# Kernel tuning notes

Measured on AMD Instinct MI355X. Metric: run time of the kernel, lower is better.

Reference implementation:

```python
import jax, jax.numpy as jnp
import numpy as np

B, D_IN, D_HID, D_OUT, N_EXP, K = 32768, 256, 512, 256, 16, 2


def setup_inputs() -> dict:
    key = jax.random.key(0)
    ks = jax.random.split(key, 5)
    s_in = 1.0 / np.sqrt(D_IN)
    s_hid = 1.0 / np.sqrt(D_HID)
    return {
        "x": jax.random.normal(ks[0], (B, D_IN), jnp.float32),
        "Wg": jax.random.normal(ks[1], (D_IN, N_EXP), jnp.float32) * s_in,
        "bg": jnp.zeros((N_EXP,), jnp.float32),
        "W1": jax.random.normal(ks[2], (N_EXP, D_IN, D_HID), jnp.float32) * s_in,
        "b1": jnp.zeros((N_EXP, D_HID), jnp.float32),
        "W2": jax.random.normal(ks[3], (N_EXP, D_HID, D_OUT), jnp.float32) * s_hid,
        "b2": jnp.zeros((N_EXP, D_OUT), jnp.float32),
    }


def reference(x, Wg, bg, W1, b1, W2, b2):
    # Gating: linear -> softmax -> top-k -> renormalize (inference path, no noise)
    logits = x @ Wg + bg                       # [B, E]
    probs = jax.nn.softmax(logits, axis=-1)
    top_w, top_idx = jax.lax.top_k(probs, K)   # [B, K]
    top_w = top_w / jnp.sum(top_w, axis=-1, keepdims=True)

    # Expert MLPs (evaluate all experts densely, then gather selected outputs;
    # same math as masked gather -> MLP -> weighted scatter-add)
    h = jax.nn.relu(jnp.einsum('bi,eih->beh', x, W1) + b1[None])  # [B, E, H]
    y_all = jnp.einsum('beh,eho->beo', h, W2) + b2[None]          # [B, E, O]

    y_sel = jnp.take_along_axis(y_all, top_idx[:, :, None], axis=1)  # [B, K, O]
    return jnp.sum(y_sel * top_w[:, :, None], axis=1)                # [B, O]
```

## Files before the change

### kernel.cpp

```cpp
#include <hip/hip_runtime.h>
#include <stdint.h>

#define BTOK 32768
#define DIN 256
#define DHID 512
#define DOUT 256
#define NEXP 16
#define BM 128
#define CH 64
#define NCH 8
#define SLOTS 96

typedef __attribute__((ext_vector_type(8))) short bf16x8;
typedef __attribute__((ext_vector_type(16))) float f32x16;

__device__ __forceinline__ unsigned short f2bf(float f){
  unsigned u = __builtin_bit_cast(unsigned, f);
  u = u + 0x7FFFu + ((u >> 16) & 1u);
  return (unsigned short)(u >> 16);
}
__device__ __forceinline__ float bf2f(unsigned short h){
  return __builtin_bit_cast(float, (unsigned)h << 16);
}
__device__ __forceinline__ void gload16(const void* g, void* l){
  __builtin_amdgcn_global_load_lds((const __attribute__((address_space(1))) unsigned int*)g,
                                   (__attribute__((address_space(3))) unsigned int*)l, 16, 0, 0);
}

__global__ __launch_bounds__(256) void transpose_cvt(const float* __restrict__ src,
                                                     unsigned short* __restrict__ dst,
                                                     int R, int C){
  __shared__ float t[32][33];
  int e = blockIdx.z, r0 = blockIdx.y * 32, c0 = blockIdx.x * 32;
  int lx = threadIdx.x & 31, ly = threadIdx.x >> 5;
  const float* s = src + (size_t)e * R * C;
  unsigned short* d = dst + (size_t)e * R * C;
#pragma unroll
  for (int i = 0; i < 4; i++){ int r = ly + i * 8; t[r][lx] = s[(size_t)(r0 + r) * C + c0 + lx]; }
  __syncthreads();
#pragma unroll
  for (int i = 0; i < 4; i++){ int r = ly + i * 8; d[(size_t)(c0 + r) * R + r0 + lx] = f2bf(t[lx][r]); }
}

__global__ __launch_bounds__(256) void transpose_cvt_w2(const float* __restrict__ src,
                                                        unsigned short* __restrict__ dst){
  __shared__ float t[32][33];
  int e = blockIdx.z, r0 = blockIdx.y * 32, c0 = blockIdx.x * 32;
  int lx = threadIdx.x & 31, ly = threadIdx.x >> 5;
  const float* s = src + (size_t)e * DHID * DOUT;
  unsigned short* d = dst + (size_t)e * DHID * DOUT + (r0 >> 6) * (DOUT * CH) + (r0 & 32);
#pragma unroll
  for (int i = 0; i < 4; i++){ int r = ly + i * 8; t[r][lx] = s[(size_t)(r0 + r) * DOUT + c0 + lx]; }
  __syncthreads();
#pragma unroll
  for (int i = 0; i < 4; i++){ int rr = ly + i * 8; d[(size_t)(c0 + rr) * CH + lx] = f2bf(t[lx][rr]); }
}

__global__ __launch_bounds__(256) void gating_kernel(const float* __restrict__ x,
                                                     const float* __restrict__ Wg,
                                                     const float* __restrict__ bg,
                                                     unsigned short* __restrict__ x_bf,
                                                     int* __restrict__ top_idx,
                                                     float* __restrict__ top_w,
                                                     int* __restrict__ counts){
  __shared__ float WgT[16][256];
  __shared__ int hist[16];
  int tid = threadIdx.x;
#pragma unroll
  for (int j = 0; j < 4; j++){
    float4 wv = *(const float4*)(Wg + tid * 16 + j * 4);
    WgT[j * 4 + 0][tid] = wv.x; WgT[j * 4 + 1][tid] = wv.y;
    WgT[j * 4 + 2][tid] = wv.z; WgT[j * 4 + 3][tid] = wv.w;
  }
  if (tid < 16) hist[tid] = 0;
  __syncthreads();
  int wid = tid >> 6, lane = tid & 63;

  for (int t = 0; t < 16; t++){
    int tok = blockIdx.x * 64 + wid * 16 + t;
    const float4 xv = *(const float4*)(x + (size_t)tok * DIN + lane * 4);
    ushort4 xb; xb.x = f2bf(xv.x); xb.y = f2bf(xv.y); xb.z = f2bf(xv.z); xb.w = f2bf(xv.w);
    *(ushort4*)(x_bf + (size_t)tok * DIN + lane * 4) = xb;
    float logit[16];
#pragma unroll
    for (int e = 0; e < 16; e++){
      const float4 wv = *(const float4*)(&WgT[e][lane * 4]);
      float v = xv.x * wv.x + xv.y * wv.y + xv.z * wv.z + xv.w * wv.w;
#pragma unroll
      for (int off = 32; off; off >>= 1) v += __shfl_xor(v, off, 64);
      logit[e] = v + bg[e];
    }
    if (lane == 0){
      int i1 = 0; float v1 = logit[0];
#pragma unroll
      for (int e = 1; e < 16; e++) if (logit[e] > v1){ v1 = logit[e]; i1 = e; }
      int i2 = -1; float v2 = -3.4e38f;
#pragma unroll
      for (int e = 0; e < 16; e++) if (e != i1 && logit[e] > v2){ v2 = logit[e]; i2 = e; }
      float tt = expf(v2 - v1);
      float w1 = 1.0f / (1.0f + tt);
      float w2 = tt / (1.0f + tt);
      top_idx[tok * 2] = i1; top_idx[tok * 2 + 1] = i2;
      top_w[tok * 2] = w1;  top_w[tok * 2 + 1] = w2;
      atomicAdd(&hist[i1], 1); atomicAdd(&hist[i2], 1);
    }
  }
  __syncthreads();
  if (tid < 16) atomicAdd(&counts[tid], hist[tid]);
}

__global__ void prefix_kernel(const int* __restrict__ counts, int* __restrict__ offsets,
                              int* __restrict__ cursor, int* __restrict__ bm_e,
                              int* __restrict__ bm_start, int* __restrict__ bm_end,
                              int* __restrict__ xcd_cnt, int* __restrict__ xcd_cur){
  int lane = threadIdx.x & 63;
  int c = (lane < 16) ? counts[lane] : 0;
  int s = c;
#pragma unroll
  for (int off = 1; off < 16; off <<= 1){ int o = __shfl_up(s, off, 64); if (lane >= off) s += o; }
  int start = s - c;
  if (lane < 16){ offsets[lane] = start; cursor[lane] = start; }
  int nb = (c + BM - 1) >> 7;
  int nb_partner = __shfl(nb, lane ^ 8, 64);
  if (lane < 8){
    int filled = nb + nb_partner;
    if (filled > SLOTS) filled = SLOTS;
    xcd_cnt[lane] = filled;
    xcd_cur[lane] = 0;
  }
  if (lane < 16){
    int sbase = (lane < 8) ? 0 : nb_partner;
    int xcd = lane & 7;
    for (int b = 0; b < nb; b++){
      int idx = xcd * SLOTS + sbase + b;
      if (sbase + b < SLOTS){
        bm_e[idx] = lane; bm_start[idx] = start + b * BM; bm_end[idx] = start + c;
      }
    }
  }
}

__global__ __launch_bounds__(256) void scatter_kernel(const int* __restrict__ top_idx,
                                                      const float* __restrict__ top_w,
                                                      int* __restrict__ cursor,
                                                      int* __restrict__ pair_tok,
                                                      float* __restrict__ pair_w){
  __shared__ int hist[16], base[16], rank[16];
  int tid = threadIdx.x;
  if (tid < 16){ hist[tid] = 0; rank[tid] = 0; }
  __syncthreads();
  int t = blockIdx.x * 256 + tid;
  int e0 = top_idx[t * 2], e1 = top_idx[t * 2 + 1];
  float w0 = top_w[t * 2], w1 = top_w[t * 2 + 1];
  atomicAdd(&hist[e0], 1); atomicAdd(&hist[e1], 1);
  __syncthreads();
  if (tid < 16) base[tid] = atomicAdd(&cursor[tid], hist[tid]);
  __syncthreads();
  int r0 = atomicAdd(&rank[e0], 1);
  int p0 = base[e0] + r0;
  pair_tok[p0] = t; pair_w[p0] = w0;
  int r1 = atomicAdd(&rank[e1], 1);
  int p1 = base[e1] + r1;
  pair_tok[p1] = t | (1 << 16); pair_w[p1] = w1;
}

__global__ __launch_bounds__(512, 1) void moe_gemm_kernel(
    const unsigned short* __restrict__ x_bf,
    const unsigned short* __restrict__ W1t,
    const unsigned short* __restrict__ W2c,
    const float* __restrict__ b1,
    const float* __restrict__ b2,
    const int* __restrict__ pair_tok, const float* __restrict__ pair_w,
    const int* __restrict__ bm_e, const int* __restrict__ bm_start,
    const int* __restrict__ bm_end,
    int* __restrict__ xcd_cur, const int* __restrict__ xcd_cnt,
    unsigned short* __restrict__ ypair){
  int xcd = blockIdx.x & 7;

  __shared__ unsigned short w1s[2][CH * 256];
  __shared__ unsigned short w2s[2][256 * CH];
  __shared__ unsigned short hs[BM * CH];
  __shared__ int s_u;

  int tid = threadIdx.x, wid = tid >> 6, lane = tid & 63;
  int l31 = lane & 31, l5 = lane >> 5;
  int mg = wid >> 1, hg = wid & 1;
  char* hsb = (char*)hs;

  int o1, o2;
  { int r = tid >> 5; o1 = r * 512 + (((tid & 31) ^ (r & 15)) * 16); }
  { int p = tid >> 4; int q = (tid & 15) ^ (p & 15);
    o2 = (p * 2 + (q >> 3)) * 128 + (q & 7) * 16; }

  int hid = hg * 32 + l31;
  int swzA = (hid & 15) << 4;
  const f32x16 fzero = {0.f,0.f,0.f,0.f,0.f,0.f,0.f,0.f,0.f,0.f,0.f,0.f,0.f,0.f,0.f,0.f};
  int cnt = xcd_cnt[xcd];

  for (;;){
    if (tid == 0) s_u = atomicAdd(&xcd_cur[xcd], 1);
    __syncthreads();
    int u = s_u;
    if (u >= cnt) break;
    int bmi = xcd * SLOTS + u;
    int e = bm_e[bmi], rs = bm_start[bmi], re = bm_end[bmi];
    const char* gW1 = (const char*)(W1t + (size_t)e * DHID * DIN);
    const char* gW2 = (const char*)(W2c + (size_t)e * DOUT * DHID);

#define STAGE(c, sl) {                                                    \
    const char* s1 = gW1 + (size_t)(c) * 32768;                           \
    const char* s2 = gW2 + (size_t)(c) * 32768;                           \
    char* d1 = (char*)w1s[sl]; char* d2 = (char*)w2s[sl];                 \
    _Pragma("unroll")                                                     \
    for (int k = 0; k < 4; k++){                                          \
      gload16(s1 + o1 + k * 8192, d1 + tid * 16 + k * 8192);              \
      gload16(s2 + o2 + k * 8192, d2 + tid * 16 + k * 8192);              \
    } }

    bf16x8 xr[16];
    {
      int g0 = rs + mg * 32 + l31;
      int gc = g0 < re ? g0 : (re - 1);
      int tok = pair_tok[gc] & 0xFFFF;
      const unsigned short* xrow = x_bf + (size_t)tok * DIN + l5 * 8;
#pragma unroll
      for (int ks = 0; ks < 16; ks++) xr[ks] = *(const bf16x8*)(xrow + ks * 16);
    }

    f32x16 acc[4];
    acc[0] = fzero; acc[1] = fzero; acc[2] = fzero; acc[3] = fzero;

    STAGE(0, 0);
    asm volatile("s_waitcnt vmcnt(0)" ::: "memory");
    __builtin_amdgcn_sched_barrier(0);
    __builtin_amdgcn_s_barrier();
    __builtin_amdgcn_sched_barrier(0);

    for (int c = 0; c < NCH; c++){
      int sl = c & 1;
      if (c + 1 < NCH) STAGE(c + 1, sl ^ 1);

      float b1v = b1[e * DHID + c * CH + hid];

      {
        const char* w1b = (const char*)w1s[sl];
        f32x16 h0 = fzero, h1 = fzero;
#pragma unroll
        for (int ks = 0; ks < 16; ks += 2){
          bf16x8 bA = *(const bf16x8*)(w1b + hid * 512 + ((ks * 32 + l5 * 16) ^ swzA));
          bf16x8 bB = *(const bf16x8*)(w1b + hid * 512 + (((ks + 1) * 32 + l5 * 16) ^ swzA));
          h0 = __builtin_amdgcn_mfma_f32_32x32x16_bf16(xr[ks], bA, h0, 0, 0, 0);
          h1 = __builtin_amdgcn_mfma_f32_32x32x16_bf16(xr[ks + 1], bB, h1, 0, 0, 0);
        }
        f32x16 hsum = h0 + h1;
        int h2 = hg * 64 + l31 * 2;
#pragma unroll
        for (int r = 0; r < 16; r++){
          int tk = mg * 32 + (r & 3) + ((r >> 2) << 3) + (l5 << 2);
          float v = fmaxf(hsum[r] + b1v, 0.f);
          int adr = (tk >> 1) * 256 + ((((tk & 1) << 7) + h2) ^ (((tk >> 1) & 15) << 4));
          *(unsigned short*)(hsb + adr) = f2bf(v);
        }
      }
      asm volatile("s_waitcnt lgkmcnt(0)" ::: "memory");
      __builtin_amdgcn_sched_barrier(0);
      __builtin_amdgcn_s_barrier();
      __builtin_amdgcn_sched_barrier(0);

      {
        const char* w2b = (const char*)w2s[sl];
        int tk = mg * 32 + l31;
        int hswz = ((tk >> 1) & 15) << 4;
        int hbase = (tk >> 1) * 256;
        int hhi = (tk & 1) << 7;
#pragma unroll
        for (int ks = 0; ks < 4; ks++){
          bf16x8 ha = *(const bf16x8*)(hsb + hbase + ((hhi + ks * 32 + l5 * 16) ^ hswz));
#pragma unroll
          for (int ot = 0; ot < 4; ot++){
            int n = hg * 128 + ot * 32 + l31;
            int adr = (n >> 1) * 256 + ((((n & 1) << 7) + ks * 32 + l5 * 16) ^ (((n >> 1) & 15) << 4));
            bf16x8 bb = *(const bf16x8*)(w2b + adr);
            acc[ot] = __builtin_amdgcn_mfma_f32_32x32x16_bf16(ha, bb, acc[ot], 0, 0, 0);
          }
        }
      }
      if (c + 1 < NCH){
        asm volatile("s_waitcnt vmcnt(0) lgkmcnt(0)" ::: "memory");
        __builtin_amdgcn_sched_barrier(0);
        __builtin_amdgcn_s_barrier();
        __builtin_amdgcn_sched_barrier(0);
      }
    }

    {
      float b2v[4];
#pragma unroll
      for (int ot = 0; ot < 4; ot++) b2v[ot] = b2[e * DOUT + hg * 128 + ot * 32 + l31];
#pragma unroll
      for (int r = 0; r < 16; r++){
        int tl = mg * 32 + (r & 3) + ((r >> 2) << 3) + (l5 << 2);
        int gg = rs + tl;
        if (gg < re){
          int pt = pair_tok[gg];
          int yrow = (pt & 0xFFFF) * 2 + (pt >> 16);
          float w = pair_w[gg];
          unsigned short* yp = ypair + (size_t)yrow * DOUT + hg * 128 + l31;
#pragma unroll
          for (int ot = 0; ot < 4; ot++)
            yp[ot * 32] = f2bf(w * (acc[ot][r] + b2v[ot]));
        }
      }
    }
#undef STAGE
  }
}

__global__ __launch_bounds__(256) void combine_kernel(const unsigned short* __restrict__ yp,
                                                      float* __restrict__ out){
  int idx = blockIdx.x * 256 + threadIdx.x;
  int t = idx >> 6;
  int c4 = (idx & 63) << 2;
  ushort4 a = *(const ushort4*)(yp + (size_t)(t * 2) * DOUT + c4);
  ushort4 b = *(const ushort4*)(yp + (size_t)(t * 2 + 1) * DOUT + c4);
  float4 o;
  o.x = bf2f(a.x) + bf2f(b.x);
  o.y = bf2f(a.y) + bf2f(b.y);
  o.z = bf2f(a.z) + bf2f(b.z);
  o.w = bf2f(a.w) + bf2f(b.w);
  *(float4*)(out + (size_t)t * DOUT + c4) = o;
}

extern "C" void kernel_launch(void* const* d_in, const int* in_sizes, int n_in,
                              void* d_out, int out_size, void* d_ws, size_t ws_size,
                              hipStream_t stream){
  (void)in_sizes; (void)n_in; (void)out_size; (void)ws_size;
  const float* x  = (const float*)d_in[0];
  const float* Wg = (const float*)d_in[1];
  const float* bg = (const float*)d_in[2];
  const float* W1 = (const float*)d_in[3];
  const float* b1 = (const float*)d_in[4];
  const float* W2 = (const float*)d_in[5];
  const float* b2 = (const float*)d_in[6];
  float* out = (float*)d_out;
  char* ws = (char*)d_ws;

  unsigned short* x_bf  = (unsigned short*)(ws);
  unsigned short* W1t   = (unsigned short*)(ws + 16777216);
  unsigned short* W2ck  = (unsigned short*)(ws + 20971520);
  unsigned short* ypair = (unsigned short*)(ws + 25165824);
  int*   top_idx  = (int*)  (ws + 58720256);
  float* top_w    = (float*)(ws + 58982400);
  int*   pair_tok = (int*)  (ws + 59244544);
  float* pair_w   = (float*)(ws + 59506688);
  int*   counts   = (int*)  (ws + 60030976);
  int*   offsets  = (int*)  (ws + 60031040);
  int*   cursor   = (int*)  (ws + 60031104);
  int*   bm_e     = (int*)  (ws + 60031232);
  int*   bm_start = (int*)  (ws + 60036608);
  int*   bm_end   = (int*)  (ws + 60041984);
  int*   xcd_cnt  = (int*)  (ws + 60045184);
  int*   xcd_cur  = (int*)  (ws + 60045248);

  hipMemsetAsync(counts, 0, 64, stream);
  transpose_cvt<<<dim3(16, 8, 16), 256, 0, stream>>>(W1, W1t, 256, 512);
  transpose_cvt_w2<<<dim3(8, 16, 16), 256, 0, stream>>>(W2, W2ck);
  gating_kernel<<<512, 256, 0, stream>>>(x, Wg, bg, x_bf, top_idx, top_w, counts);
  prefix_kernel<<<1, 64, 0, stream>>>(counts, offsets, cursor, bm_e, bm_start, bm_end,
                                      xcd_cnt, xcd_cur);
  scatter_kernel<<<128, 256, 0, stream>>>(top_idx, top_w, cursor, pair_tok, pair_w);
  moe_gemm_kernel<<<256, 512, 0, stream>>>(x_bf, W1t, W2ck, b1, b2, pair_tok, pair_w,
                                           bm_e, bm_start, bm_end, xcd_cur, xcd_cnt, ypair);
  combine_kernel<<<8192, 256, 0, stream>>>(ypair, out);
}
```

Baseline: 158.5 us.

## Halve hidden chunk size and run two 256-thread blocks per CU in MoE GEMM

Shrinks the hidden-dimension chunk from 64 to 32 (16 chunks instead of 8), halving the LDS used by the weight and hidden staging buffers so two 256-thread blocks can share a CU. Each wave now owns a full 32-token row group and all 256 output columns, which doubles its output accumulators to 8 MFMA tiles. The W2 pre-layout and the LDS swizzles are reworked for the 32-wide chunk, and b1 is cached once per block in LDS. The trade-off is more barriers per tile and higher register pressure, in exchange for more resident waves to overlap latency.

```diff
diff --git a/kernel.cpp b/kernel.cpp
--- a/kernel.cpp
+++ b/kernel.cpp
@@ -7,8 +7,8 @@
 #define DOUT 256
 #define NEXP 16
 #define BM 128
-#define CH 64
-#define NCH 8
+#define CH 32
+#define NCH 16
 #define SLOTS 96
 
 typedef __attribute__((ext_vector_type(8))) short bf16x8;
@@ -48,7 +48,7 @@
   int e = blockIdx.z, r0 = blockIdx.y * 32, c0 = blockIdx.x * 32;
   int lx = threadIdx.x & 31, ly = threadIdx.x >> 5;
   const float* s = src + (size_t)e * DHID * DOUT;
-  unsigned short* d = dst + (size_t)e * DHID * DOUT + (r0 >> 6) * (DOUT * CH) + (r0 & 32);
+  unsigned short* d = dst + (size_t)e * DHID * DOUT + (r0 >> 5) * (DOUT * CH);
 #pragma unroll
   for (int i = 0; i < 4; i++){ int r = ly + i * 8; t[r][lx] = s[(size_t)(r0 + r) * DOUT + c0 + lx]; }
   __syncthreads();
@@ -164,7 +164,7 @@
   pair_tok[p1] = t | (1 << 16); pair_w[p1] = w1;
 }
 
-__global__ __launch_bounds__(512, 1) void moe_gemm_kernel(
+__global__ __launch_bounds__(256, 2) void moe_gemm_kernel(
     const unsigned short* __restrict__ x_bf,
     const unsigned short* __restrict__ W1t,
     const unsigned short* __restrict__ W2c,
@@ -180,19 +180,15 @@
   __shared__ unsigned short w1s[2][CH * 256];
   __shared__ unsigned short w2s[2][256 * CH];
   __shared__ unsigned short hs[BM * CH];
+  __shared__ float b1s[DHID];
   __shared__ int s_u;
 
   int tid = threadIdx.x, wid = tid >> 6, lane = tid & 63;
   int l31 = lane & 31, l5 = lane >> 5;
-  int mg = wid >> 1, hg = wid & 1;
+  int mg = wid;
   char* hsb = (char*)hs;
 
-  int o1, o2;
-  { int r = tid >> 5; o1 = r * 512 + (((tid & 31) ^ (r & 15)) * 16); }
-  { int p = tid >> 4; int q = (tid & 15) ^ (p & 15);
-    o2 = (p * 2 + (q >> 3)) * 128 + (q & 7) * 16; }
-
-  int hid = hg * 32 + l31;
+  int hid = l31;
   int swzA = (hid & 15) << 4;
   const f32x16 fzero = {0.f,0.f,0.f,0.f,0.f,0.f,0.f,0.f,0.f,0.f,0.f,0.f,0.f,0.f,0.f,0.f};
   int cnt = xcd_cnt[xcd];
@@ -208,14 +204,22 @@
     const char* gW2 = (const char*)(W2c + (size_t)e * DOUT * DHID);
 
 #define STAGE(c, sl) {                                                    \
-    const char* s1 = gW1 + (size_t)(c) * 32768;                           \
-    const char* s2 = gW2 + (size_t)(c) * 32768;                           \
+    const char* s1 = gW1 + (size_t)(c) * 16384;                           \
+    const char* s2 = gW2 + (size_t)(c) * 16384;                           \
     char* d1 = (char*)w1s[sl]; char* d2 = (char*)w2s[sl];                 \
     _Pragma("unroll")                                                     \
     for (int k = 0; k < 4; k++){                                          \
-      gload16(s1 + o1 + k * 8192, d1 + tid * 16 + k * 8192);              \
-      gload16(s2 + o2 + k * 8192, d2 + tid * 16 + k * 8192);              \
+      int g = k * 256 + tid;                                              \
+      int r_ = g >> 5;                                                    \
+      int of1 = r_ * 512 + (((g & 31) ^ (r_ & 15)) * 16);                 \
+      int p_ = g >> 3, q_ = (g & 7) ^ (p_ & 7);                           \
+      int of2 = (p_ * 2 + (q_ >> 2)) * 64 + (q_ & 3) * 16;                \
+      gload16(s1 + of1, d1 + g * 16);                                     \
+      gload16(s2 + of2, d2 + g * 16);                                     \
     } }
+
+    b1s[tid] = b1[e * DHID + tid];
+    b1s[tid + 256] = b1[e * DHID + 256 + tid];
 
     bf16x8 xr[16];
     {
@@ -227,8 +231,9 @@
       for (int ks = 0; ks < 16; ks++) xr[ks] = *(const bf16x8*)(xrow + ks * 16);
     }
 
-    f32x16 acc[4];
-    acc[0] = fzero; acc[1] = fzero; acc[2] = fzero; acc[3] = fzero;
+    f32x16 acc[8];
+#pragma unroll
+    for (int i = 0; i < 8; i++) acc[i] = fzero;
 
     STAGE(0, 0);
     asm volatile("s_waitcnt vmcnt(0)" ::: "memory");
@@ -239,8 +244,6 @@
     for (int c = 0; c < NCH; c++){
       int sl = c & 1;
       if (c + 1 < NCH) STAGE(c + 1, sl ^ 1);
-
-      float b1v = b1[e * DHID + c * CH + hid];
 
       {
         const char* w1b = (const char*)w1s[sl];
@@ -253,12 +256,12 @@
           h1 = __builtin_amdgcn_mfma_f32_32x32x16_bf16(xr[ks + 1], bB, h1, 0, 0, 0);
         }
         f32x16 hsum = h0 + h1;
-        int h2 = hg * 64 + l31 * 2;
+        float b1v = b1s[c * CH + l31];
 #pragma unroll
         for (int r = 0; r < 16; r++){
           int tk = mg * 32 + (r & 3) + ((r >> 2) << 3) + (l5 << 2);
           float v = fmaxf(hsum[r] + b1v, 0.f);
-          int adr = (tk >> 1) * 256 + ((((tk & 1) << 7) + h2) ^ (((tk >> 1) & 15) << 4));
+          int adr = (tk >> 1) * 128 + ((((tk & 1) << 6) + l31 * 2) ^ (((tk >> 1) & 7) << 4));
           *(unsigned short*)(hsb + adr) = f2bf(v);
         }
       }
@@ -270,18 +273,19 @@
       {
         const char* w2b = (const char*)w2s[sl];
         int tk = mg * 32 + l31;
-        int hswz = ((tk >> 1) & 15) << 4;
-        int hbase = (tk >> 1) * 256;
-        int hhi = (tk & 1) << 7;
-#pragma unroll
-        for (int ks = 0; ks < 4; ks++){
-          bf16x8 ha = *(const bf16x8*)(hsb + hbase + ((hhi + ks * 32 + l5 * 16) ^ hswz));
-#pragma unroll
-          for (int ot = 0; ot < 4; ot++){
-            int n = hg * 128 + ot * 32 + l31;
-            int adr = (n >> 1) * 256 + ((((n & 1) << 7) + ks * 32 + l5 * 16) ^ (((n >> 1) & 15) << 4));
-            bf16x8 bb = *(const bf16x8*)(w2b + adr);
-            acc[ot] = __builtin_amdgcn_mfma_f32_32x32x16_bf16(ha, bb, acc[ot], 0, 0, 0);
+        int hb = (tk >> 1) * 128, hswz = ((tk >> 1) & 7) << 4, hhi = (tk & 1) << 6;
+        bf16x8 ha[2];
+#pragma unroll
+        for (int ks = 0; ks < 2; ks++)
+          ha[ks] = *(const bf16x8*)(hsb + hb + ((hhi + ks * 32 + l5 * 16) ^ hswz));
+#pragma unroll
+        for (int ot = 0; ot < 8; ot++){
+          int n = ot * 32 + l31;
+          int nb_ = (n >> 1) * 128, nswz = ((n >> 1) & 7) << 4, nhi = (n & 1) << 6;
+#pragma unroll
+          for (int ks = 0; ks < 2; ks++){
+            bf16x8 bb = *(const bf16x8*)(w2b + nb_ + ((nhi + ks * 32 + l5 * 16) ^ nswz));
+            acc[ot] = __builtin_amdgcn_mfma_f32_32x32x16_bf16(ha[ks], bb, acc[ot], 0, 0, 0);
           }
         }
       }
@@ -294,9 +298,9 @@
     }
 
     {
-      float b2v[4];
-#pragma unroll
-      for (int ot = 0; ot < 4; ot++) b2v[ot] = b2[e * DOUT + hg * 128 + ot * 32 + l31];
+      float b2v[8];
+#pragma unroll
+      for (int ot = 0; ot < 8; ot++) b2v[ot] = b2[e * DOUT + ot * 32 + l31];
 #pragma unroll
       for (int r = 0; r < 16; r++){
         int tl = mg * 32 + (r & 3) + ((r >> 2) << 3) + (l5 << 2);
@@ -305,9 +309,9 @@
           int pt = pair_tok[gg];
           int yrow = (pt & 0xFFFF) * 2 + (pt >> 16);
           float w = pair_w[gg];
-          unsigned short* yp = ypair + (size_t)yrow * DOUT + hg * 128 + l31;
-#pragma unroll
-          for (int ot = 0; ot < 4; ot++)
+          unsigned short* yp = ypair + (size_t)yrow * DOUT + l31;
+#pragma unroll
+          for (int ot = 0; ot < 8; ot++)
             yp[ot * 32] = f2bf(w * (acc[ot][r] + b2v[ot]));
         }
       }
@@ -369,7 +373,7 @@
   prefix_kernel<<<1, 64, 0, stream>>>(counts, offsets, cursor, bm_e, bm_start, bm_end,
                                       xcd_cnt, xcd_cur);
   scatter_kernel<<<128, 256, 0, stream>>>(top_idx, top_w, cursor, pair_tok, pair_w);
-  moe_gemm_kernel<<<256, 512, 0, stream>>>(x_bf, W1t, W2ck, b1, b2, pair_tok, pair_w,
+  moe_gemm_kernel<<<512, 256, 0, stream>>>(x_bf, W1t, W2ck, b1, b2, pair_tok, pair_w,
                                            bm_e, bm_start, bm_end, xcd_cur, xcd_cnt, ypair);
   combine_kernel<<<8192, 256, 0, stream>>>(ypair, out);
 }
```

Result: slower. 227.9 us (+43.8%).
